# Performance work log

Hardware: AMD Instinct MI355X
Metric: run time of the kernel (lower is better)

## Reference

```python
import jax, jax.numpy as jnp
import numpy as np
from jax import lax

N_KERNELS = 10000
IN_CH = 3
BATCH = 64
T_LEN = 1024
KSIZES = [7, 9, 11]
DILS = [1, 2, 4, 8, 16]
MAXK = max(KSIZES)

# Deterministic stand-in for torch's random per-kernel (size, dilation) draw.
_rng = np.random.default_rng(0)
_ks = np.array(KSIZES)[_rng.integers(0, len(KSIZES), N_KERNELS)]
_dil = np.array(DILS)[_rng.integers(0, len(DILS), N_KERNELS)]
GROUPS = []  # (kernel_size, dilation, static index array)
for _k in KSIZES:
    for _d in DILS:
        _idx = np.nonzero((_ks == _k) & (_dil == _d))[0]
        if _idx.size:
            GROUPS.append((_k, _d, _idx))
_PERM = np.concatenate([g[2] for g in GROUPS])  # grouped order -> original kernel id
INV_PERM = np.argsort(_PERM)                    # restore original kernel order


def setup_inputs() -> dict:
    key = jax.random.key(0)
    kx, kw, kb = jax.random.split(key, 3)
    x = jax.random.normal(kx, (BATCH, IN_CH, T_LEN), dtype=jnp.float32)
    # Weights padded to MAXK taps; taps beyond each kernel's size are zeroed
    # (zero taps do not change the conv output within the valid window).
    w = jax.random.normal(kw, (N_KERNELS, IN_CH, MAXK), dtype=jnp.float32)
    tap_mask = (np.arange(MAXK)[None, :] < _ks[:, None]).astype(np.float32)
    weights = w * jnp.asarray(tap_mask)[:, None, :]
    biases = 0.1 * jax.random.normal(kb, (N_KERNELS,), dtype=jnp.float32)
    return {"x": x, "weights": weights, "biases": biases}


def _rocket(x, weights, biases):
    # Group kernels by (size, dilation) -> <=15 batched convs instead of 10000 tiny ones.
    maxs, ppvs = [], []
    for k, d, idx in GROUPS:
        w = weights[idx, :, :k]                 # (G, C, k), idx is a static np array
        pad = (k - 1) * d // 2                  # 'same' padding (k odd -> exact)
        out = lax.conv_general_dilated(
            x, w, window_strides=(1,), padding=[(pad, pad)],
            rhs_dilation=(d,), dimension_numbers=("NCH", "OIH", "NCH"))
        out = out + biases[idx][None, :, None]  # (B, G, T)
        maxs.append(out.max(-1))                             # max pooling feature
        ppvs.append((out > 0).astype(jnp.float32).mean(-1))  # PPV feature
    mx = jnp.concatenate(maxs, 1)[:, INV_PERM]  # (B, N) in original kernel order
    pv = jnp.concatenate(ppvs, 1)[:, INV_PERM]
    # Interleave [max_0, ppv_0, max_1, ppv_1, ...] like torch.stack(features, dim=1)
    return jnp.stack([mx, pv], -1).reshape(x.shape[0], 2 * N_KERNELS)


def reference(x, weights, biases):
    return _rocket(x, weights, biases)
```

## Files before the change

### kernel.cpp

```cpp
#include <hip/hip_runtime.h>
#include <stdint.h>

#define N_KERNELS 10000
#define NCHUNK 56
#define CH_ALLOC 1312

typedef unsigned __int128 u128;
typedef __attribute__((ext_vector_type(8)))  short short8;
typedef __attribute__((ext_vector_type(16))) float floatx16;
typedef __attribute__((ext_vector_type(4)))  unsigned int uint4v;
typedef __attribute__((ext_vector_type(2)))  unsigned int uint2v;

struct KDraws { uint8_t k[N_KERNELS]; uint8_t d[N_KERNELS]; };

constexpr KDraws make_kd() {
    KDraws kd{};
    const u128 MULT = (((u128)0x2360ED051FC65DA4ULL) << 64) | 0x4385DF649FCCF645ULL;

    uint32_t hc = 0x43b0d7e5u;
    uint32_t pool[4] = {};
    for (int i = 0; i < 4; i++) {
        uint32_t v = 0u;
        v ^= hc; hc *= 0x931e8875u;
        v *= hc; v ^= v >> 16;
        pool[i] = v;
    }
    for (int s = 0; s < 4; s++)
        for (int dd = 0; dd < 4; dd++)
            if (s != dd) {
                uint32_t hv = pool[s];
                hv ^= hc; hc *= 0x931e8875u;
                hv *= hc; hv ^= hv >> 16;
                uint32_t rr = 0xca01f9ddu * pool[dd] - 0x4973f715u * hv;
                rr ^= rr >> 16;
                pool[dd] = rr;
            }
    uint32_t st[8] = {};
    uint32_t hcb = 0x8b51f9ddu;
    for (int i = 0; i < 8; i++) {
        uint32_t dv = pool[i & 3];
        dv ^= hcb; hcb *= 0x58f38dedu;
        dv *= hcb; dv ^= dv >> 16;
        st[i] = dv;
    }
    uint64_t w0 = (uint64_t)st[0] | ((uint64_t)st[1] << 32);
    uint64_t w1 = (uint64_t)st[2] | ((uint64_t)st[3] << 32);
    uint64_t w2 = (uint64_t)st[4] | ((uint64_t)st[5] << 32);
    uint64_t w3 = (uint64_t)st[6] | ((uint64_t)st[7] << 32);
    u128 initstate = (((u128)w0) << 64) | w1;
    u128 initseq   = (((u128)w2) << 64) | w3;

    u128 inc   = (initseq << 1) | 1;
    u128 state = 0;
    state = state * MULT + inc;
    state += initstate;
    state = state * MULT + inc;

    u128 s = state;
    for (int t = 0; t < 10000; ++t) {
        s = s * MULT + inc;
        uint64_t hi = (uint64_t)(s >> 64), lo = (uint64_t)s;
        unsigned rot = (unsigned)(hi >> 58);
        uint64_t v = hi ^ lo;
        uint64_t o = (v >> rot) | (v << ((64u - rot) & 63u));
        uint32_t d0 = (uint32_t)o;
        uint32_t d1 = (uint32_t)(o >> 32);
        int i0 = 2 * t, i1 = 2 * t + 1;
        if (i0 < 10000) kd.k[i0] = (uint8_t)(((uint64_t)d0 * 3u) >> 32);
        else            kd.d[i0 - 10000] = (uint8_t)(((uint64_t)d0 * 5u) >> 32);
        if (i1 < 10000) kd.k[i1] = (uint8_t)(((uint64_t)d1 * 3u) >> 32);
        else            kd.d[i1 - 10000] = (uint8_t)(((uint64_t)d1 * 5u) >> 32);
    }
    return kd;
}

constexpr KDraws kdr = make_kd();

struct Tables {
    alignas(16) int sched[4 * NCHUNK];
    int list[N_KERNELS];
};

constexpr Tables make_tables(const KDraws& kd) {
    Tables T{};
    int cnt[15] = {}, off[15] = {}, cur[15] = {};
    for (int i = 0; i < 10000; ++i) cnt[(int)kd.k[i] * 5 + (int)kd.d[i]]++;
    int o = 0;
    for (int g = 0; g < 15; ++g) { off[g] = o; cur[g] = o; o += cnt[g]; }
    for (int i = 0; i < 10000; ++i) {
        int g = (int)kd.k[i] * 5 + (int)kd.d[i];
        T.list[cur[g]++] = i;
    }
    const int kv[3] = {7, 9, 11};
    int ci = 0;
    for (int g = 0; g < 15; ++g) {
        int sz = cnt[g];
        for (int s2 = 0; s2 < sz; s2 += 256) {
            T.sched[4 * ci + 0] = kv[g / 5];
            T.sched[4 * ci + 1] = g % 5;
            T.sched[4 * ci + 2] = off[g] + s2;
            T.sched[4 * ci + 3] = (sz - s2 < 256) ? (sz - s2) : 256;
            ci++;
        }
    }
    for (; ci < NCHUNK; ci++) {
        T.sched[4 * ci + 0] = 0; T.sched[4 * ci + 1] = 0;
        T.sched[4 * ci + 2] = 0; T.sched[4 * ci + 3] = 0;
    }
    return T;
}

__constant__ Tables g_T = make_tables(kdr);

__device__ __forceinline__ uint16_t f32_to_bf16(float v) {
    uint32_t u = __builtin_bit_cast(uint32_t, v);
    return (uint16_t)((u + 0x7FFFu + ((u >> 16) & 1u)) >> 16);
}

__device__ __forceinline__ void stat16t(const floatx16& C, float& mx, int& cnt,
                                        float nb) {
    float g0 = fmaxf(fmaxf(C[0],  C[1]),  C[2]);
    float g1 = fmaxf(fmaxf(C[3],  C[4]),  C[5]);
    float g2 = fmaxf(fmaxf(C[6],  C[7]),  C[8]);
    float g3 = fmaxf(fmaxf(C[9],  C[10]), C[11]);
    float g4 = fmaxf(fmaxf(C[12], C[13]), C[14]);
    float h0 = fmaxf(fmaxf(g0, g1), g2);
    float h1 = fmaxf(fmaxf(g3, g4), C[15]);
    mx = fmaxf(mx, fmaxf(h0, h1));
    #pragma unroll
    for (int i = 0; i < 16; ++i)
        cnt += (C[i] > nb) ? 1 : 0;
}

template <int K, int D>
__device__ __forceinline__ void body(const float* __restrict__ x,
                                     const float* __restrict__ wgt,
                                     const float* __restrict__ bias,
                                     int lstart, int valid,
                                     float* __restrict__ out,
                                     short* __restrict__ xs,
                                     int b) {
    constexpr int H = (K - 1) / 2;
    constexpr int Q = 1024 / D;
    constexpr int S = Q + 16;
    constexpr int O = (8 - H) & 7;

    const int tid   = threadIdx.x;
    const int lane  = tid & 63;
    const int wave  = tid >> 6;
    const int jbase = (lane >> 5) * 8;
    const int m31   = lane & 31;

    for (int idx = tid; idx < 3 * CH_ALLOC; idx += 256) {
        int c = idx / CH_ALLOC;
        int P = idx - c * CH_ALLOC;
        float v = 0.f;
        int y = P - 8;
        if (y >= 0) {
            int r = y / S;
            int q = y - r * S;
            if (r < D && q < Q) v = x[((size_t)b * 3 + c) * 1024 + r + D * q];
        }
        xs[idx] = (short)f32_to_bf16(v);
    }

    int i0 = wave * 64 + m31;
    int i1 = i0 + 32;
    int n0 = g_T.list[lstart + (i0 < valid ? i0 : valid - 1)];
    int n1 = g_T.list[lstart + (i1 < valid ? i1 : valid - 1)];
    short8 whi[2][3];
    #pragma unroll
    for (int t2 = 0; t2 < 2; ++t2) {
        int n = t2 ? n1 : n0;
        #pragma unroll
        for (int c = 0; c < 3; ++c) {
            #pragma unroll
            for (int u = 0; u < 8; ++u) {
                int j = jbase + u;
                float wv = (j < 11) ? wgt[n * 33 + c * 11 + j] : 0.f;
                whi[t2][c][u] = (short)f32_to_bf16(wv);
            }
        }
    }
    float bv0 = bias[n0], bv1 = bias[n1];
    float nb0 = -bv0, nb1 = -bv1;

    const floatx16 Zv = (floatx16)0.0f;

    __syncthreads();

    float mx0 = -3.402823466e38f, mx1 = -3.402823466e38f;
    int cnt0 = 0, cnt1 = 0;

    #pragma unroll 1
    for (int ri = 0; ri < 4; ++ri) {
        int rb, qb;
        if constexpr (D == 1)      { rb = 0;                   qb = 256 * ri + 8 * m31; }
        else if constexpr (D == 2) { rb = ri >> 1;             qb = (ri & 1) * 256 + 8 * m31; }
        else if constexpr (D == 4) { rb = ri;                  qb = 8 * m31; }
        else if constexpr (D == 8) { rb = 2 * ri + (m31 >> 4); qb = 8 * (m31 & 15); }
        else                       { rb = 4 * ri + (m31 >> 3); qb = 8 * (m31 & 7); }
        int Bm    = 8 - H + rb * S + qb;
        int rbase = (Bm - O) + jbase;

        uint32_t w[3][10];
        #pragma unroll
        for (int c = 0; c < 3; ++c) {
            const short* bp = xs + c * CH_ALLOC + rbase;
            uint4v u0 = *reinterpret_cast<const uint4v*>(bp);
            uint4v u1 = *reinterpret_cast<const uint4v*>(bp + 8);
            uint2v u2 = *reinterpret_cast<const uint2v*>(bp + 16);
            w[c][0] = u0[0]; w[c][1] = u0[1]; w[c][2] = u0[2]; w[c][3] = u0[3];
            w[c][4] = u1[0]; w[c][5] = u1[1]; w[c][6] = u1[2]; w[c][7] = u1[3];
            w[c][8] = u2[0]; w[c][9] = u2[1];
        }

        #pragma unroll
        for (int p = 0; p < 8; ++p) {
            const int s = O + p;
            const int j = s >> 1;
            short8 A0, A1, A2;
            #pragma unroll
            for (int c = 0; c < 3; ++c) {
                uint4v t;
                if (s & 1) {
                    t[0] = (w[c][j]     >> 16) | (w[c][j + 1] << 16);
                    t[1] = (w[c][j + 1] >> 16) | (w[c][j + 2] << 16);
                    t[2] = (w[c][j + 2] >> 16) | (w[c][j + 3] << 16);
                    t[3] = (w[c][j + 3] >> 16) | (w[c][j + 4] << 16);
                } else {
                    t[0] = w[c][j];     t[1] = w[c][j + 1];
                    t[2] = w[c][j + 2]; t[3] = w[c][j + 3];
                }
                short8 Ac = __builtin_bit_cast(short8, t);
                if (c == 0) A0 = Ac; else if (c == 1) A1 = Ac; else A2 = Ac;
            }
            floatx16 C0, C1;
            C0 = __builtin_amdgcn_mfma_f32_32x32x16_bf16(A0, whi[0][0], Zv, 0, 0, 0);
            C1 = __builtin_amdgcn_mfma_f32_32x32x16_bf16(A0, whi[1][0], Zv, 0, 0, 0);
            C0 = __builtin_amdgcn_mfma_f32_32x32x16_bf16(A1, whi[0][1], C0, 0, 0, 0);
            C1 = __builtin_amdgcn_mfma_f32_32x32x16_bf16(A1, whi[1][1], C1, 0, 0, 0);
            C0 = __builtin_amdgcn_mfma_f32_32x32x16_bf16(A2, whi[0][2], C0, 0, 0, 0);
            C1 = __builtin_amdgcn_mfma_f32_32x32x16_bf16(A2, whi[1][2], C1, 0, 0, 0);
            stat16t(C0, mx0, cnt0, nb0);
            stat16t(C1, mx1, cnt1, nb1);
        }
    }

    mx0  = fmaxf(mx0, __shfl_xor(mx0, 32));
    mx1  = fmaxf(mx1, __shfl_xor(mx1, 32));
    cnt0 += __shfl_xor(cnt0, 32);
    cnt1 += __shfl_xor(cnt1, 32);

    if (lane < 32) {
        float2* ob = reinterpret_cast<float2*>(out + (size_t)b * (2 * N_KERNELS));
        ob[n0] = make_float2(mx0 + bv0, (float)cnt0 * (1.0f / 1024.0f));
        ob[n1] = make_float2(mx1 + bv1, (float)cnt1 * (1.0f / 1024.0f));
    }
}

__global__ __launch_bounds__(256, 4)
void rocket_main(const float* __restrict__ x, const float* __restrict__ wgt,
                 const float* __restrict__ bias, float* __restrict__ out) {
    __shared__ __align__(16) short xs[3 * CH_ALLOC];
    int kc     = g_T.sched[4 * blockIdx.x + 0];
    int ld2    = g_T.sched[4 * blockIdx.x + 1];
    int lstart = g_T.sched[4 * blockIdx.x + 2];
    int valid  = g_T.sched[4 * blockIdx.x + 3];
    if (valid == 0) return;
    int b = blockIdx.y;
    switch (kc * 8 + ld2) {
        case 7*8+0:  body<7, 1 >(x, wgt, bias, lstart, valid, out, xs, b); break;
        case 7*8+1:  body<7, 2 >(x, wgt, bias, lstart, valid, out, xs, b); break;
        case 7*8+2:  body<7, 4 >(x, wgt, bias, lstart, valid, out, xs, b); break;
        case 7*8+3:  body<7, 8 >(x, wgt, bias, lstart, valid, out, xs, b); break;
        case 7*8+4:  body<7, 16>(x, wgt, bias, lstart, valid, out, xs, b); break;
        case 9*8+0:  body<9, 1 >(x, wgt, bias, lstart, valid, out, xs, b); break;
        case 9*8+1:  body<9, 2 >(x, wgt, bias, lstart, valid, out, xs, b); break;
        case 9*8+2:  body<9, 4 >(x, wgt, bias, lstart, valid, out, xs, b); break;
        case 9*8+3:  body<9, 8 >(x, wgt, bias, lstart, valid, out, xs, b); break;
        case 9*8+4:  body<9, 16>(x, wgt, bias, lstart, valid, out, xs, b); break;
        case 11*8+0: body<11,1 >(x, wgt, bias, lstart, valid, out, xs, b); break;
        case 11*8+1: body<11,2 >(x, wgt, bias, lstart, valid, out, xs, b); break;
        case 11*8+2: body<11,4 >(x, wgt, bias, lstart, valid, out, xs, b); break;
        case 11*8+3: body<11,8 >(x, wgt, bias, lstart, valid, out, xs, b); break;
        default:     body<11,16>(x, wgt, bias, lstart, valid, out, xs, b); break;
    }
}

extern "C" void kernel_launch(void* const* d_in, const int* in_sizes, int n_in,
                              void* d_out, int out_size, void* d_ws, size_t ws_size,
                              hipStream_t stream) {
    const float* x   = (const float*)d_in[0];
    const float* w   = (const float*)d_in[1];
    const float* b   = (const float*)d_in[2];
    float* out = (float*)d_out;
    (void)d_ws; (void)ws_size;

    hipLaunchKernelGGL(rocket_main, dim3(NCHUNK, 64), dim3(256), 0, stream,
                       x, w, b, out);
}
```

Measured before the change: 156.8 us.

## Stage phase-shifted LDS copies, fold bias into MFMA, use sign-bit counting

The input slab is now written to shared memory four times at 2-element phase offsets, so each tap position reads aligned 16-byte vectors straight from LDS instead of holding a register window and shifting it per tap. The bias is folded into the matmul through an extra weight slot paired with a constant-one input lane, so the positive count becomes a sign-bit sum and the max needs no bias add afterwards. The launch grid is trimmed to the real number of schedule chunks so no blocks exit empty. In exchange LDS per block grows about fourfold, which may lower occupancy, and the bias now goes through bf16 rounding.

```diff
diff --git a/kernel.cpp b/kernel.cpp
--- a/kernel.cpp
+++ b/kernel.cpp
@@ -4,12 +4,12 @@
 #define N_KERNELS 10000
 #define NCHUNK 56
 #define CH_ALLOC 1312
+#define PP_STRIDE (3 * CH_ALLOC)
 
 typedef unsigned __int128 u128;
 typedef __attribute__((ext_vector_type(8)))  short short8;
 typedef __attribute__((ext_vector_type(16))) float floatx16;
 typedef __attribute__((ext_vector_type(4)))  unsigned int uint4v;
-typedef __attribute__((ext_vector_type(2)))  unsigned int uint2v;
 
 struct KDraws { uint8_t k[N_KERNELS]; uint8_t d[N_KERNELS]; };
 
@@ -112,13 +112,22 @@
 
 __constant__ Tables g_T = make_tables(kdr);
 
+constexpr int count_chunks() {
+    int cnt[15] = {};
+    for (int i = 0; i < 10000; ++i) cnt[(int)kdr.k[i] * 5 + (int)kdr.d[i]]++;
+    int ci = 0;
+    for (int g = 0; g < 15; ++g)
+        for (int s2 = 0; s2 < cnt[g]; s2 += 256) ci++;
+    return ci;
+}
+constexpr int NCHUNK_REAL = count_chunks();
+
 __device__ __forceinline__ uint16_t f32_to_bf16(float v) {
     uint32_t u = __builtin_bit_cast(uint32_t, v);
     return (uint16_t)((u + 0x7FFFu + ((u >> 16) & 1u)) >> 16);
 }
 
-__device__ __forceinline__ void stat16t(const floatx16& C, float& mx, int& cnt,
-                                        float nb) {
+__device__ __forceinline__ void stat16(const floatx16& C, float& mx, int& cnt) {
     float g0 = fmaxf(fmaxf(C[0],  C[1]),  C[2]);
     float g1 = fmaxf(fmaxf(C[3],  C[4]),  C[5]);
     float g2 = fmaxf(fmaxf(C[6],  C[7]),  C[8]);
@@ -128,8 +137,11 @@
     float h1 = fmaxf(fmaxf(g3, g4), C[15]);
     mx = fmaxf(mx, fmaxf(h0, h1));
     #pragma unroll
-    for (int i = 0; i < 16; ++i)
-        cnt += (C[i] > nb) ? 1 : 0;
+    for (int i = 0; i < 16; i += 2) {
+        int s0 = __builtin_bit_cast(int, C[i])     >> 31;
+        int s1 = __builtin_bit_cast(int, C[i + 1]) >> 31;
+        cnt += s0 + s1;
+    }
 }
 
 template <int K, int D>
@@ -140,20 +152,21 @@
                                      float* __restrict__ out,
                                      short* __restrict__ xs,
                                      int b) {
-    constexpr int H = (K - 1) / 2;
-    constexpr int Q = 1024 / D;
-    constexpr int S = Q + 16;
-    constexpr int O = (8 - H) & 7;
+    constexpr int H  = (K - 1) / 2;
+    constexpr int Q  = 1024 / D;
+    constexpr int S  = Q + 16;
+    constexpr int OB = 8 - H;
 
     const int tid   = threadIdx.x;
     const int lane  = tid & 63;
     const int wave  = tid >> 6;
     const int jbase = (lane >> 5) * 8;
     const int m31   = lane & 31;
-
-    for (int idx = tid; idx < 3 * CH_ALLOC; idx += 256) {
-        int c = idx / CH_ALLOC;
-        int P = idx - c * CH_ALLOC;
+    const bool hi   = (jbase == 8);
+
+    for (int idx = tid; idx < 3 * (CH_ALLOC + 8); idx += 256) {
+        int c = idx / (CH_ALLOC + 8);
+        int P = idx - c * (CH_ALLOC + 8);
         float v = 0.f;
         int y = P - 8;
         if (y >= 0) {
@@ -161,36 +174,55 @@
             int q = y - r * S;
             if (r < D && q < Q) v = x[((size_t)b * 3 + c) * 1024 + r + D * q];
         }
-        xs[idx] = (short)f32_to_bf16(v);
+        short hv = (short)f32_to_bf16(v);
+        #pragma unroll
+        for (int ph = 0; ph < 4; ++ph) {
+            int ee = P - 2 * ph;
+            if (ee >= 0 && ee < CH_ALLOC)
+                xs[ph * PP_STRIDE + c * CH_ALLOC + ee] = hv;
+        }
     }
 
     int i0 = wave * 64 + m31;
     int i1 = i0 + 32;
     int n0 = g_T.list[lstart + (i0 < valid ? i0 : valid - 1)];
     int n1 = g_T.list[lstart + (i1 < valid ? i1 : valid - 1)];
+    float bv0 = bias[n0], bv1 = bias[n1];
     short8 whi[2][3];
     #pragma unroll
     for (int t2 = 0; t2 < 2; ++t2) {
         int n = t2 ? n1 : n0;
+        float bv = t2 ? bv1 : bv0;
         #pragma unroll
         for (int c = 0; c < 3; ++c) {
             #pragma unroll
             for (int u = 0; u < 8; ++u) {
                 int j = jbase + u;
                 float wv = (j < 11) ? wgt[n * 33 + c * 11 + j] : 0.f;
+                if (c == 2 && u == 7 && hi) wv = bv;
                 whi[t2][c][u] = (short)f32_to_bf16(wv);
             }
         }
     }
-    float bv0 = bias[n0], bv1 = bias[n1];
-    float nb0 = -bv0, nb1 = -bv1;
 
     const floatx16 Zv = (floatx16)0.0f;
+    const short one_bf16 = (short)0x3F80;
 
     __syncthreads();
 
     float mx0 = -3.402823466e38f, mx1 = -3.402823466e38f;
     int cnt0 = 0, cnt1 = 0;
+
+    auto oddload = [](const short* cp) -> short8 {
+        uint4v dv = __builtin_bit_cast(uint4v, *reinterpret_cast<const short8*>(cp));
+        uint32_t d4 = *reinterpret_cast<const uint32_t*>(cp + 8);
+        uint4v t;
+        t[0] = (dv[0] >> 16) | (dv[1] << 16);
+        t[1] = (dv[1] >> 16) | (dv[2] << 16);
+        t[2] = (dv[2] >> 16) | (dv[3] << 16);
+        t[3] = (dv[3] >> 16) | (d4    << 16);
+        return __builtin_bit_cast(short8, t);
+    };
 
     #pragma unroll 1
     for (int ri = 0; ri < 4; ++ri) {
@@ -200,41 +232,27 @@
         else if constexpr (D == 4) { rb = ri;                  qb = 8 * m31; }
         else if constexpr (D == 8) { rb = 2 * ri + (m31 >> 4); qb = 8 * (m31 & 15); }
         else                       { rb = 4 * ri + (m31 >> 3); qb = 8 * (m31 & 7); }
-        int Bm    = 8 - H + rb * S + qb;
-        int rbase = (Bm - O) + jbase;
-
-        uint32_t w[3][10];
-        #pragma unroll
-        for (int c = 0; c < 3; ++c) {
-            const short* bp = xs + c * CH_ALLOC + rbase;
-            uint4v u0 = *reinterpret_cast<const uint4v*>(bp);
-            uint4v u1 = *reinterpret_cast<const uint4v*>(bp + 8);
-            uint2v u2 = *reinterpret_cast<const uint2v*>(bp + 16);
-            w[c][0] = u0[0]; w[c][1] = u0[1]; w[c][2] = u0[2]; w[c][3] = u0[3];
-            w[c][4] = u1[0]; w[c][5] = u1[1]; w[c][6] = u1[2]; w[c][7] = u1[3];
-            w[c][8] = u2[0]; w[c][9] = u2[1];
-        }
+        const int Abase = OB + rb * S + qb + jbase;
 
         #pragma unroll
         for (int p = 0; p < 8; ++p) {
-            const int s = O + p;
-            const int j = s >> 1;
+            const int o8  = (OB + p) & 7;
+            const bool od = (o8 & 1) != 0;
+            const int ph  = (od ? o8 - 1 : o8) >> 1;
+            const int L   = Abase + (p - o8);
+            const short* bp = xs + ph * PP_STRIDE + L;
             short8 A0, A1, A2;
-            #pragma unroll
-            for (int c = 0; c < 3; ++c) {
-                uint4v t;
-                if (s & 1) {
-                    t[0] = (w[c][j]     >> 16) | (w[c][j + 1] << 16);
-                    t[1] = (w[c][j + 1] >> 16) | (w[c][j + 2] << 16);
-                    t[2] = (w[c][j + 2] >> 16) | (w[c][j + 3] << 16);
-                    t[3] = (w[c][j + 3] >> 16) | (w[c][j + 4] << 16);
-                } else {
-                    t[0] = w[c][j];     t[1] = w[c][j + 1];
-                    t[2] = w[c][j + 2]; t[3] = w[c][j + 3];
-                }
-                short8 Ac = __builtin_bit_cast(short8, t);
-                if (c == 0) A0 = Ac; else if (c == 1) A1 = Ac; else A2 = Ac;
+            if (!od) {
+                A0 = *reinterpret_cast<const short8*>(bp);
+                A1 = *reinterpret_cast<const short8*>(bp + CH_ALLOC);
+                A2 = *reinterpret_cast<const short8*>(bp + 2 * CH_ALLOC);
+            } else {
+                A0 = oddload(bp);
+                A1 = oddload(bp + CH_ALLOC);
+                A2 = oddload(bp + 2 * CH_ALLOC);
             }
+            A2[7] = hi ? one_bf16 : A2[7];
+
             floatx16 C0, C1;
             C0 = __builtin_amdgcn_mfma_f32_32x32x16_bf16(A0, whi[0][0], Zv, 0, 0, 0);
             C1 = __builtin_amdgcn_mfma_f32_32x32x16_bf16(A0, whi[1][0], Zv, 0, 0, 0);
@@ -242,8 +260,8 @@
             C1 = __builtin_amdgcn_mfma_f32_32x32x16_bf16(A1, whi[1][1], C1, 0, 0, 0);
             C0 = __builtin_amdgcn_mfma_f32_32x32x16_bf16(A2, whi[0][2], C0, 0, 0, 0);
             C1 = __builtin_amdgcn_mfma_f32_32x32x16_bf16(A2, whi[1][2], C1, 0, 0, 0);
-            stat16t(C0, mx0, cnt0, nb0);
-            stat16t(C1, mx1, cnt1, nb1);
+            stat16(C0, mx0, cnt0);
+            stat16(C1, mx1, cnt1);
         }
     }
 
@@ -254,15 +272,15 @@
 
     if (lane < 32) {
         float2* ob = reinterpret_cast<float2*>(out + (size_t)b * (2 * N_KERNELS));
-        ob[n0] = make_float2(mx0 + bv0, (float)cnt0 * (1.0f / 1024.0f));
-        ob[n1] = make_float2(mx1 + bv1, (float)cnt1 * (1.0f / 1024.0f));
+        ob[n0] = make_float2(mx0, (float)(1024 + cnt0) * (1.0f / 1024.0f));
+        ob[n1] = make_float2(mx1, (float)(1024 + cnt1) * (1.0f / 1024.0f));
     }
 }
 
 __global__ __launch_bounds__(256, 4)
 void rocket_main(const float* __restrict__ x, const float* __restrict__ wgt,
                  const float* __restrict__ bias, float* __restrict__ out) {
-    __shared__ __align__(16) short xs[3 * CH_ALLOC];
+    __shared__ __align__(16) short xs[4 * PP_STRIDE];
     int kc     = g_T.sched[4 * blockIdx.x + 0];
     int ld2    = g_T.sched[4 * blockIdx.x + 1];
     int lstart = g_T.sched[4 * blockIdx.x + 2];
@@ -297,6 +315,6 @@
     float* out = (float*)d_out;
     (void)d_ws; (void)ws_size;
 
-    hipLaunchKernelGGL(rocket_main, dim3(NCHUNK, 64), dim3(256), 0, stream,
+    hipLaunchKernelGGL(rocket_main, dim3(NCHUNK_REAL, 64), dim3(256), 0, stream,
                        x, w, b, out);
 }
```

After: 131.9 us. 1.19x faster.
